# Performance work log

Hardware: AMD Instinct MI355X
Metric: run time of the kernel (lower is better)

The kernel has to match this reference:

```python
import jax, jax.numpy as jnp
import numpy as np

PSEUDO3D = True
DO_TUBE = True
DILATION_ITERATIONS = 1

# Neighbor offsets P2..P9 (clockwise from north), as in Zhang-Suen / skimage skeletonize
_OFFS = [(-1, 0), (-1, 1), (0, 1), (1, 1), (1, 0), (1, -1), (0, -1), (-1, -1)]


def _shift(a, dy, dx):
    # out[n, y, x] = a[n, y+dy, x+dx], zero-padded borders (same as skimage's 0-pad)
    N, H, W = a.shape
    p = jnp.pad(a, ((0, 0), (1, 1), (1, 1)))
    return p[:, 1 + dy:1 + dy + H, 1 + dx:1 + dx + W]


def _subiter(img, first):
    # One Zhang-Suen sub-iteration on a stack of 2D slices [N, H, W] (bool)
    P = [_shift(img, dy, dx) for dy, dx in _OFFS]
    B = sum(p.astype(jnp.int32) for p in P)            # nonzero-neighbor count
    seq = P + [P[0]]
    A = sum(((~seq[k]) & seq[k + 1]).astype(jnp.int32) for k in range(8))  # 0->1 transitions
    P2, P3, P4, P5, P6, P7, P8, P9 = P
    if first:
        c = (~(P2 & P4 & P6)) & (~(P4 & P6 & P8))
    else:
        c = (~(P2 & P4 & P8)) & (~(P2 & P6 & P8))
    remove = img & (B >= 2) & (B <= 6) & (A == 1) & c
    return img & ~remove


def _thin_stack(stack):
    # Zhang-Suen thinning of every 2D slice in a [N, H, W] bool stack, run to convergence.
    # All slices are processed in one while_loop; converged slices are fixed points, so
    # extra iterations are no-ops and the result matches per-slice skeletonize.
    def body(state):
        img, _ = state
        new = _subiter(_subiter(img, True), False)
        return new, jnp.any(new != img)

    def cond(state):
        return state[1]

    img, _ = jax.lax.while_loop(cond, body, (stack, jnp.array(True)))
    return img


def _dilate6(v):
    # scipy.ndimage.binary_dilation with the default 6-connected 3D structure, border 0
    D, H, W = v.shape
    p = jnp.pad(v, 1)
    out = v
    for dz, dy, dx in [(1, 0, 0), (-1, 0, 0), (0, 1, 0), (0, -1, 0), (0, 0, 1), (0, 0, -1)]:
        out = out | p[1 + dz:1 + dz + D, 1 + dy:1 + dy + H, 1 + dx:1 + dx + W]
    return out


def setup_inputs() -> dict:
    key = jax.random.key(0)
    gt = jax.random.randint(key, (1, 48, 384, 384), 0, 2).astype(jnp.float32)
    return {"gt_skel": gt}


def reference(gt_skel):
    vol = gt_skel[0]                      # squeeze(axis=0) -> [D, H, W]
    mask = vol == 1.0                     # bool
    skel = _thin_stack(mask)              # per z-slice skeletonize
    if PSEUDO3D:
        # per y-slice: mask[:, y, :] has shape [D, W]
        skel = skel | jnp.transpose(_thin_stack(jnp.transpose(mask, (1, 0, 2))), (1, 0, 2))
        # per x-slice: mask[:, :, x] has shape [D, H]
        skel = skel | jnp.transpose(_thin_stack(jnp.transpose(mask, (2, 0, 1))), (1, 2, 0))
    if DO_TUBE:
        for _ in range(DILATION_ITERATIONS):
            skel = _dilate6(skel)
    skel = skel & mask                    # skel &= gt_skel.astype(bool) (values are 0/1)
    return skel[None].astype(jnp.float32)
```

## Files before the change

kernel.cpp:

```cpp
#include <hip/hip_runtime.h>

typedef unsigned long long u64;

constexpr int D = 48, H = 384, W = 384;
constexpr int WPR = 6;
constexpr int NVOX = D * H * W;
constexpr int NWVOL = D * H * WPR;
constexpr int MPAD = 40;

__device__ __forceinline__ void fa(u64 a, u64 b, u64 c, u64& s, u64& cy) {
  u64 x = a ^ b;
  s = x ^ c;
  cy = (a & b) | (c & x);
}

template<int R>
__device__ __forceinline__ u64 zs_word(const u64* buf, int idx, int r, int wc, bool first) {
  const u64 img = buf[idx];
  if (!img) return 0;
  u64 w00 = 0, w01 = 0, w02 = 0, w10 = 0, w12 = 0, w20 = 0, w21 = 0, w22 = 0;
  const u64 w11 = img;
  const bool rm = (r > 0), rp = (r < R - 1);
  const bool cm = (wc > 0), cp = (wc < WPR - 1);
  if (rm) {
    w01 = buf[idx - WPR];
    if (cm) w00 = buf[idx - WPR - 1];
    if (cp) w02 = buf[idx - WPR + 1];
  }
  if (cm) w10 = buf[idx - 1];
  if (cp) w12 = buf[idx + 1];
  if (rp) {
    w21 = buf[idx + WPR];
    if (cm) w20 = buf[idx + WPR - 1];
    if (cp) w22 = buf[idx + WPR + 1];
  }
  const u64 P2 = w01;
  const u64 P3 = (w01 >> 1) | (w02 << 63);
  const u64 P4 = (w11 >> 1) | (w12 << 63);
  const u64 P5 = (w21 >> 1) | (w22 << 63);
  const u64 P6 = w21;
  const u64 P7 = (w21 << 1) | (w20 >> 63);
  const u64 P8 = (w11 << 1) | (w10 >> 63);
  const u64 P9 = (w01 << 1) | (w00 >> 63);

  u64 s1, c1, s2, c2, s3, c3, u0, u1, v1, v2;
  fa(P2, P3, P4, s1, c1);
  fa(P5, P6, P7, s2, c2);
  fa(P8, P9, 0ull, s3, c3);
  fa(s1, s2, s3, u0, u1);
  fa(c1, c2, c3, v1, v2);
  u64 b1 = u1 ^ v1, k2 = u1 & v1;
  u64 b2 = v2 ^ k2, b3 = v2 & k2;
  u64 condB = (b1 | b2 | b3) & ~(b3 | (b2 & b1 & u0));

  u64 t0 = ~P2 & P3, t1 = ~P3 & P4, t2 = ~P4 & P5, t3 = ~P5 & P6;
  u64 t4 = ~P6 & P7, t5 = ~P7 & P8, t6 = ~P8 & P9, t7 = ~P9 & P2;
  fa(t0, t1, t2, s1, c1);
  fa(t3, t4, t5, s2, c2);
  fa(t6, t7, 0ull, s3, c3);
  fa(s1, s2, s3, u0, u1);
  fa(c1, c2, c3, v1, v2);
  u64 a1 = u1 ^ v1, j2 = u1 & v1;
  u64 a2 = v2 ^ j2, a3 = v2 & j2;
  u64 condA = u0 & ~(a1 | a2 | a3);

  u64 cc = first ? ((~(P2 & P4 & P6)) & (~(P4 & P6 & P8)))
                 : ((~(P2 & P4 & P8)) & (~(P2 & P6 & P8)));
  return img & ~(condB & condA & cc);
}

__device__ __forceinline__ bool dirty3(const u64* U, int q) {
  const int pb = q + 64;
  const int w = pb >> 6, sh = pb & 63;
  u64 v = U[w] >> sh;
  if (sh > 61) v |= U[w + 1] << (64 - sh);
  return (v & 7ull) != 0;
}

template<int R, bool FIRST>
__device__ __forceinline__ void subpass(const u64* __restrict__ src, u64* __restrict__ dst,
                                        u64* rawW, const u64* rawPrev,
                                        u64* Uw, const u64* Ur,
                                        int* chgflag, int tid, int nthr) {
  constexpr int NW = R * WPR;
  int anych = 0;
  for (int base = 0; base < NW; base += nthr) {
    const int idx = base + tid;
    int changed = 0;
    if (idx < NW) {
      const int r = idx / WPR, wc = idx - r * WPR;
      const u64 old = src[idx];
      u64 nw = old;
      const bool dirty = dirty3(Ur, idx - 1)
                       | dirty3(Ur, idx - WPR - 1)
                       | dirty3(Ur, idx + WPR - 1);
      if (dirty) {
        nw = zs_word<R>(src, idx, r, wc, FIRST);
        changed = (nw != old);
      }
      dst[idx] = nw;
      anych |= changed;
    }
    const u64 bal = __ballot(changed != 0);
    if ((tid & 63) == 0 && idx < NW) {
      const int mw = 1 + (idx >> 6);
      rawW[mw] = bal;
      Uw[mw] = bal | rawPrev[mw];
    }
  }
  if (anych) *chgflag = 1;
}

template<int R, int MODE>
__device__ __forceinline__ void thin_body(const u64* __restrict__ maskP,
                                          u64* __restrict__ skelZY,
                                          u64* __restrict__ skelX,
                                          int slice, u64* Abuf, u64* Bbuf,
                                          u64 (*raw)[MPAD], u64 (*Um)[MPAD],
                                          int* s_chg) {
  constexpr int NW = R * WPR;
  constexpr int MW = (NW + 63) >> 6;
  const int tid = threadIdx.x;
  const int nthr = blockDim.x;

  if (MODE == 0) {
    for (int idx = tid; idx < NW; idx += nthr) {
      int r = idx / WPR, wc = idx - r * WPR;
      Abuf[idx] = maskP[(slice * H + r) * WPR + wc];
    }
  } else if (MODE == 1) {
    for (int idx = tid; idx < NW; idx += nthr) {
      int r = idx / WPR, wc = idx - r * WPR;
      Abuf[idx] = maskP[(r * H + slice) * WPR + wc];
    }
  } else {
    const int lane = tid & 63, wave = tid >> 6, nwv = nthr >> 6;
    const int xw = slice >> 6, xb = slice & 63;
    for (int idx = wave; idx < NW; idx += nwv) {
      int r = idx / WPR, wc = idx - r * WPR;
      int c = wc * 64 + lane;
      u64 bit = (maskP[(r * H + c) * WPR + xw] >> xb) & 1ull;
      u64 w = __ballot(bit != 0);
      if (lane == 0) Abuf[idx] = w;
    }
  }

  for (int t = tid; t < 4 * MPAD; t += nthr) {
    const int arr = t / MPAD, j = t - arr * MPAD;
    const u64 v = (j >= 1 && j <= MW) ? ~0ull : 0ull;
    if (arr < 2) raw[arr][j] = v; else Um[arr - 2][j] = v;
  }
  if (tid < 2) s_chg[tid] = 0;
  __syncthreads();

  int p = 0;
  while (true) {
    if (tid == 0) s_chg[p ^ 1] = 0;
    subpass<R, true >(Abuf, Bbuf, raw[0], raw[1], Um[0], Um[1], &s_chg[p], tid, nthr);
    __syncthreads();
    subpass<R, false>(Bbuf, Abuf, raw[1], raw[0], Um[1], Um[0], &s_chg[p], tid, nthr);
    __syncthreads();
    const int stop = (s_chg[p] == 0);
    p ^= 1;
    __syncthreads();
    if (stop) break;
  }

  for (int idx = tid; idx < NW; idx += nthr) {
    u64 w = Abuf[idx];
    if (!w) continue;
    int r = idx / WPR, wc = idx - r * WPR;
    if (MODE == 0)      atomicOr(&skelZY[(slice * H + r) * WPR + wc], w);
    else if (MODE == 1) atomicOr(&skelZY[(r * H + slice) * WPR + wc], w);
    else                skelX[(r * W + slice) * WPR + wc] = w;
  }
}

__global__ __launch_bounds__(1024) void thin_all(const u64* __restrict__ maskP,
                                                 u64* __restrict__ skelZY,
                                                 u64* __restrict__ skelX) {
  __shared__ u64 Abuf[H * WPR];
  __shared__ u64 Bbuf[H * WPR];
  __shared__ u64 raw[2][MPAD];
  __shared__ u64 Um[2][MPAD];
  __shared__ int s_chg[2];
  const int b = blockIdx.x;
  if (b < D) {
    thin_body<H, 0>(maskP, skelZY, skelX, b, Abuf, Bbuf, raw, Um, s_chg);
  } else if (b < D + H) {
    thin_body<D, 1>(maskP, skelZY, skelX, b - D, Abuf, Bbuf, raw, Um, s_chg);
  } else {
    thin_body<D, 2>(maskP, skelZY, skelX, b - D - H, Abuf, Bbuf, raw, Um, s_chg);
  }
}

__global__ void init_pack(const float* __restrict__ in, u64* __restrict__ maskP,
                          u64* __restrict__ skelZY, u64* __restrict__ skelX) {
  const int lane = threadIdx.x & 63;
  const int gwave = (blockIdx.x * blockDim.x + threadIdx.x) >> 6;
  const int nwaves = (gridDim.x * blockDim.x) >> 6;
  for (int widx = gwave; widx < NWVOL; widx += nwaves) {
    float v = in[(size_t)widx * 64 + lane];
    u64 w = __ballot(v == 1.0f);
    if (lane == 0) {
      maskP[widx] = w;
      skelZY[widx] = 0;
      skelX[widx] = 0;
    }
  }
}

__global__ void transpose_or(const u64* __restrict__ skelX,
                             u64* __restrict__ skelZY) {
  const int gw = (blockIdx.x * blockDim.x + threadIdx.x) >> 6;
  const int lane = threadIdx.x & 63;
  const int z = gw / 36, rem = gw - z * 36;
  const int yw = rem / 6, xw = rem - yw * 6;
  const int x = xw * 64 + lane;
  const u64 wx = skelX[(z * W + x) * WPR + yw];
  u64 mine = 0;
  #pragma unroll 8
  for (int j = 0; j < 64; ++j) {
    u64 wj = __ballot((wx >> j) & 1ull);
    if (lane == j) mine = wj;
  }
  const int y = yw * 64 + lane;
  if (mine) skelZY[(z * H + y) * WPR + xw] |= mine;
}

__global__ void dilate_expand(const u64* __restrict__ maskP,
                              const u64* __restrict__ skelZY,
                              float* __restrict__ out) {
  const int idx = blockIdx.x * blockDim.x + threadIdx.x;
  if (idx >= NVOX / 4) return;
  const int i4 = idx * 4;
  const int wi = i4 >> 6;
  const int wc = wi % WPR;
  const int row = wi / WPR;
  const int y = row % H;
  const int z = row / H;

  const u64 S = skelZY[wi];
  const u64 L = (wc > 0) ? skelZY[wi - 1] : 0ull;
  const u64 Rw = (wc < WPR - 1) ? skelZY[wi + 1] : 0ull;
  u64 d = S | (S << 1) | (L >> 63) | (S >> 1) | (Rw << 63);
  if (y > 0)     d |= skelZY[wi - WPR];
  if (y < H - 1) d |= skelZY[wi + WPR];
  if (z > 0)     d |= skelZY[wi - H * WPR];
  if (z < D - 1) d |= skelZY[wi + H * WPR];
  const u64 r = d & maskP[wi];

  const int sh = i4 & 63;
  float4 o;
  o.x = (float)((r >> (sh + 0)) & 1ull);
  o.y = (float)((r >> (sh + 1)) & 1ull);
  o.z = (float)((r >> (sh + 2)) & 1ull);
  o.w = (float)((r >> (sh + 3)) & 1ull);
  *reinterpret_cast<float4*>(out + i4) = o;
}

extern "C" void kernel_launch(void* const* d_in, const int* in_sizes, int n_in,
                              void* d_out, int out_size, void* d_ws, size_t ws_size,
                              hipStream_t stream) {
  const float* in = (const float*)d_in[0];
  float* out = (float*)d_out;
  u64* wsw = (u64*)d_ws;
  u64* maskP = wsw;
  u64* skelZY = wsw + NWVOL;
  u64* skelX = wsw + 2 * NWVOL;

  init_pack<<<864, 256, 0, stream>>>(in, maskP, skelZY, skelX);
  thin_all<<<D + H + W, 1024, 0, stream>>>(maskP, skelZY, skelX);
  transpose_or<<<(NWVOL + 255) / 256, 256, 0, stream>>>(skelX, skelZY);
  dilate_expand<<<(NVOX / 4 + 255) / 256, 256, 0, stream>>>(maskP, skelZY, out);
}
```

Before: 72.29 us.

## Scatter x-slice skeleton bits directly via atomics, drop transpose kernel

The x-slice thinning results are now written into the ZY skeleton with one bitwise atomicOr per set voxel, replacing the intermediate skelX buffer and the separate transpose_or kernel. The per-iteration convergence check drops one __syncthreads by resetting the alternate change flag between subpasses. init_pack gets twice as many blocks and no longer zeroes skelX. This removes a kernel launch and a buffer pass, but adds many scattered per-bit atomics to global memory for the 384 x-slice blocks.

```diff
diff --git a/kernel.cpp b/kernel.cpp
--- a/kernel.cpp
+++ b/kernel.cpp
@@ -114,7 +114,6 @@
 template<int R, int MODE>
 __device__ __forceinline__ void thin_body(const u64* __restrict__ maskP,
                                           u64* __restrict__ skelZY,
-                                          u64* __restrict__ skelX,
                                           int slice, u64* Abuf, u64* Bbuf,
                                           u64 (*raw)[MPAD], u64 (*Um)[MPAD],
                                           int* s_chg) {
@@ -153,32 +152,42 @@
   if (tid < 2) s_chg[tid] = 0;
   __syncthreads();
 
-  int p = 0;
+  int k = 0;
   while (true) {
-    if (tid == 0) s_chg[p ^ 1] = 0;
-    subpass<R, true >(Abuf, Bbuf, raw[0], raw[1], Um[0], Um[1], &s_chg[p], tid, nthr);
+    subpass<R, true >(Abuf, Bbuf, raw[0], raw[1], Um[0], Um[1], &s_chg[k], tid, nthr);
     __syncthreads();
-    subpass<R, false>(Bbuf, Abuf, raw[1], raw[0], Um[1], Um[0], &s_chg[p], tid, nthr);
+    if (tid == 0) s_chg[k ^ 1] = 0;
+    subpass<R, false>(Bbuf, Abuf, raw[1], raw[0], Um[1], Um[0], &s_chg[k], tid, nthr);
     __syncthreads();
-    const int stop = (s_chg[p] == 0);
-    p ^= 1;
-    __syncthreads();
-    if (stop) break;
-  }
-
-  for (int idx = tid; idx < NW; idx += nthr) {
-    u64 w = Abuf[idx];
-    if (!w) continue;
-    int r = idx / WPR, wc = idx - r * WPR;
-    if (MODE == 0)      atomicOr(&skelZY[(slice * H + r) * WPR + wc], w);
-    else if (MODE == 1) atomicOr(&skelZY[(r * H + slice) * WPR + wc], w);
-    else                skelX[(r * W + slice) * WPR + wc] = w;
+    if (s_chg[k] == 0) break;
+    k ^= 1;
+  }
+
+  if (MODE == 2) {
+    const int xw = slice >> 6;
+    const u64 xbit = 1ull << (slice & 63);
+    for (int idx = tid; idx < NW; idx += nthr) {
+      u64 w = Abuf[idx];
+      const int z = idx / WPR, yw = idx - z * WPR;
+      while (w) {
+        const int b = __builtin_ctzll(w);
+        w &= w - 1;
+        atomicOr(&skelZY[(z * H + (yw * 64 + b)) * WPR + xw], xbit);
+      }
+    }
+  } else {
+    for (int idx = tid; idx < NW; idx += nthr) {
+      u64 w = Abuf[idx];
+      if (!w) continue;
+      int r = idx / WPR, wc = idx - r * WPR;
+      if (MODE == 0) atomicOr(&skelZY[(slice * H + r) * WPR + wc], w);
+      else           atomicOr(&skelZY[(r * H + slice) * WPR + wc], w);
+    }
   }
 }
 
 __global__ __launch_bounds__(1024) void thin_all(const u64* __restrict__ maskP,
-                                                 u64* __restrict__ skelZY,
-                                                 u64* __restrict__ skelX) {
+                                                 u64* __restrict__ skelZY) {
   __shared__ u64 Abuf[H * WPR];
   __shared__ u64 Bbuf[H * WPR];
   __shared__ u64 raw[2][MPAD];
@@ -186,16 +195,16 @@
   __shared__ int s_chg[2];
   const int b = blockIdx.x;
   if (b < D) {
-    thin_body<H, 0>(maskP, skelZY, skelX, b, Abuf, Bbuf, raw, Um, s_chg);
+    thin_body<H, 0>(maskP, skelZY, b, Abuf, Bbuf, raw, Um, s_chg);
   } else if (b < D + H) {
-    thin_body<D, 1>(maskP, skelZY, skelX, b - D, Abuf, Bbuf, raw, Um, s_chg);
+    thin_body<D, 1>(maskP, skelZY, b - D, Abuf, Bbuf, raw, Um, s_chg);
   } else {
-    thin_body<D, 2>(maskP, skelZY, skelX, b - D - H, Abuf, Bbuf, raw, Um, s_chg);
+    thin_body<D, 2>(maskP, skelZY, b - D - H, Abuf, Bbuf, raw, Um, s_chg);
   }
 }
 
 __global__ void init_pack(const float* __restrict__ in, u64* __restrict__ maskP,
-                          u64* __restrict__ skelZY, u64* __restrict__ skelX) {
+                          u64* __restrict__ skelZY) {
   const int lane = threadIdx.x & 63;
   const int gwave = (blockIdx.x * blockDim.x + threadIdx.x) >> 6;
   const int nwaves = (gridDim.x * blockDim.x) >> 6;
@@ -205,27 +214,8 @@
     if (lane == 0) {
       maskP[widx] = w;
       skelZY[widx] = 0;
-      skelX[widx] = 0;
-    }
-  }
-}
-
-__global__ void transpose_or(const u64* __restrict__ skelX,
-                             u64* __restrict__ skelZY) {
-  const int gw = (blockIdx.x * blockDim.x + threadIdx.x) >> 6;
-  const int lane = threadIdx.x & 63;
-  const int z = gw / 36, rem = gw - z * 36;
-  const int yw = rem / 6, xw = rem - yw * 6;
-  const int x = xw * 64 + lane;
-  const u64 wx = skelX[(z * W + x) * WPR + yw];
-  u64 mine = 0;
-  #pragma unroll 8
-  for (int j = 0; j < 64; ++j) {
-    u64 wj = __ballot((wx >> j) & 1ull);
-    if (lane == j) mine = wj;
-  }
-  const int y = yw * 64 + lane;
-  if (mine) skelZY[(z * H + y) * WPR + xw] |= mine;
+    }
+  }
 }
 
 __global__ void dilate_expand(const u64* __restrict__ maskP,
@@ -267,10 +257,8 @@
   u64* wsw = (u64*)d_ws;
   u64* maskP = wsw;
   u64* skelZY = wsw + NWVOL;
-  u64* skelX = wsw + 2 * NWVOL;
-
-  init_pack<<<864, 256, 0, stream>>>(in, maskP, skelZY, skelX);
-  thin_all<<<D + H + W, 1024, 0, stream>>>(maskP, skelZY, skelX);
-  transpose_or<<<(NWVOL + 255) / 256, 256, 0, stream>>>(skelX, skelZY);
+
+  init_pack<<<1728, 256, 0, stream>>>(in, maskP, skelZY);
+  thin_all<<<D + H + W, 1024, 0, stream>>>(maskP, skelZY);
   dilate_expand<<<(NVOX / 4 + 255) / 256, 256, 0, stream>>>(maskP, skelZY, out);
 }
```

Measured after the change: 174.8 us. 142% more time.
